# Kernel tuning notes

Measured on AMD Instinct MI355X. Metric: run time of the kernel, lower is better.

The kernel has to match this reference:

```python
import jax, jax.numpy as jnp
import numpy as np

N = 8192      # nodes (N_features)
D = 64        # oscillator dimension
E_K = 262144  # Kuramoto coupling edges
E_HK = 262144 # Hopfield-Kuramoto coupling edges
H = 64        # interaction MLP hidden width (N_weights)
KAPPA_K = 2.0
KAPPA_H = 2.0


def setup_inputs() -> dict:
    key = jax.random.key(0)
    ks = jax.random.split(key, 9)
    return dict(
        state_H=jax.random.normal(ks[0], (N,), dtype=jnp.float32),
        state_K=jax.random.normal(ks[1], (N, D), dtype=jnp.float32),
        W_H=jax.random.normal(ks[2], (N, N), dtype=jnp.float32) / np.float32(np.sqrt(N)),
        omega=jax.random.normal(ks[3], (D, D), dtype=jnp.float32),
        w1=jax.random.normal(ks[4], (1, H), dtype=jnp.float32),
        b1=jnp.zeros((H,), dtype=jnp.float32),
        w2=jax.random.normal(ks[5], (H, 1), dtype=jnp.float32) / np.float32(np.sqrt(H)),
        ind_K=jax.random.randint(ks[6], (E_K, 2), 0, N),
        ind_HK=jax.random.randint(ks[7], (E_HK, 2), 0, N),
    )


def _interaction_K(s, w1, b1, w2):
    # edgewise scalar MLP: [E] -> [E], dE/ds of the Kuramoto interaction energy
    h = jnp.tanh(s[:, None] @ w1 + b1)  # [E, H]
    return (h @ w2)[:, 0]               # [E]


def reference(state_H, state_K, W_H, omega, w1, b1, w2, ind_K, ind_HK):
    # normalize oscillator states onto unit sphere (per node)
    state_K = state_K / jnp.linalg.norm(state_K, axis=1, keepdims=True)

    i, j = ind_HK[:, 0], ind_HK[:, 1]
    Gram = jnp.sum(state_K[i] * state_K[j], axis=1)  # [E_HK]

    # Hopfield model: g = LNet.get_g(state_H), f_H = Hopfield_model(t, state_H, ...)
    g = jnp.tanh(state_H)                 # [N]
    f_H = -state_H + W_H @ g              # [N] dense Hopfield dynamics
    f_H = f_H.at[i].add(Gram * g[j] / KAPPA_H)
    f_H = f_H.at[j].add(Gram * g[i] / KAPPA_H)

    # Kuramoto edge coupling
    p, q = ind_K[:, 0], ind_K[:, 1]
    s = jnp.sum(state_K[p] * state_K[q], axis=1)        # [E_K]
    dE_ds = _interaction_K(s, w1, b1, w2)[:, None]      # [E_K, 1]
    f_K = jnp.zeros_like(state_K)
    f_K = f_K.at[p].add(dE_ds * state_K[q])
    f_K = f_K.at[q].add(dE_ds * state_K[p])

    # Hopfield->Kuramoto coupling
    G = (g[i] * g[j])[:, None]                          # [E_HK, 1]
    f_K = f_K.at[i].add(-G * state_K[j] / KAPPA_K)
    f_K = f_K.at[j].add(-G * state_K[i] / KAPPA_K)

    # project onto tangent of the sphere + antisymmetric rotation
    f_K = (-f_K
           + state_K * jnp.sum(state_K * f_K, axis=1, keepdims=True)
           + state_K @ ((omega - omega.T) * 0.5))
    return (f_H, f_K)
```

## Files before the change

kernel.cpp:

```cpp
#include <hip/hip_runtime.h>
#include <math.h>

#define N 8192
#define D 64
#define E_K 262144
#define E_HK 262144
#define NEDGE (E_K + E_HK)
#define CAP 256
#define TAB_N 2048

__device__ inline float fast_tanh(float x) {
  x = fminf(15.f, fmaxf(-15.f, x));
  float e = __expf(2.f * x);
  return (e - 1.f) * __builtin_amdgcn_rcpf(e + 1.f);
}

__device__ inline float wave_reduce(float v) {
  #pragma unroll
  for (int off = 32; off > 0; off >>= 1) v += __shfl_xor(v, off);
  return v;
}

__global__ __launch_bounds__(256) void prep_scatter_kernel(
    const float* __restrict__ state_K, const float* __restrict__ state_H,
    const float* __restrict__ omega,
    const int* __restrict__ ind_HK, const int* __restrict__ ind_K,
    const float* __restrict__ w1, const float* __restrict__ b1,
    const float* __restrict__ w2,
    float* __restrict__ Knorm, float* __restrict__ g, float* __restrict__ Om,
    float* __restrict__ Tab, int* __restrict__ cursor,
    unsigned* __restrict__ entries) {
  int b = blockIdx.x;
  if (b < 2048) {
    int t = b * 256 + threadIdx.x;
    int2 e = (t < E_HK) ? ((const int2*)ind_HK)[t]
                        : ((const int2*)ind_K)[t - E_HK];
    unsigned i = (unsigned)e.x, j = (unsigned)e.y;
    int s0 = atomicAdd(&cursor[i], 1);
    if (s0 < CAP) entries[i * CAP + s0] = (j << 19) | (unsigned)t;
    int s1 = atomicAdd(&cursor[j], 1);
    if (s1 < CAP) entries[j * CAP + s1] = (i << 19) | (unsigned)t;
  } else if (b < 4096) {
    int lane = threadIdx.x & 63;
    int row  = (b - 2048) * 4 + (threadIdx.x >> 6);
    float v  = state_K[row * D + lane];
    float ss = wave_reduce(v * v);
    Knorm[row * D + lane] = v * __builtin_amdgcn_rcpf(sqrtf(ss));
    if (lane == 0) g[row] = fast_tanh(state_H[row]);
  } else if (b == 4096) {
    for (int t = threadIdx.x; t < D * D; t += 256) {
      int a = t >> 6, c = t & 63;
      Om[t] = 0.5f * (omega[a * D + c] - omega[c * D + a]);
    }
  } else {
    int lane = threadIdx.x & 63;
    int p = (b - 4097) * 4 + (threadIdx.x >> 6);
    if (p <= TAB_N) {
      float s = (float)p * (2.0f / TAB_N) - 1.0f;
      float t = fast_tanh(s * w1[lane] + b1[lane]) * w2[lane];
      t = wave_reduce(t);
      if (lane == 0) Tab[p] = t;
    }
  }
}

__global__ __launch_bounds__(256) void matvec_coeff_kernel(
    const float* __restrict__ W_H, const float* __restrict__ g,
    const float* __restrict__ state_H, const float* __restrict__ Knorm,
    const float* __restrict__ Tab,
    const int* __restrict__ ind_HK, const int* __restrict__ ind_K,
    float* __restrict__ f_H, float* __restrict__ coeff) {
  int b    = blockIdx.x;
  int lane = threadIdx.x & 63;
  int wv   = threadIdx.x >> 6;
  __shared__ float sbuf[4];
  if (b < N) {
    int row = b;
    const float4* Wrow = reinterpret_cast<const float4*>(W_H + (size_t)row * N);
    const float4* g4   = reinterpret_cast<const float4*>(g);
    float acc = 0.0f;
    #pragma unroll
    for (int c = threadIdx.x; c < N / 4; c += 256) {
      float4 w = Wrow[c];
      float4 gg = g4[c];
      acc += w.x * gg.x + w.y * gg.y + w.z * gg.z + w.w * gg.w;
    }
    acc = wave_reduce(acc);
    if (lane == 0) sbuf[wv] = acc;
    __syncthreads();
    if (threadIdx.x == 0)
      f_H[row] = -state_H[row] + sbuf[0] + sbuf[1] + sbuf[2] + sbuf[3];
  } else {
    int wid = (b - N) * 4 + wv;
    int2 e = (wid < E_HK) ? ((const int2*)ind_HK)[wid]
                          : ((const int2*)ind_K)[wid - E_HK];
    float kp = Knorm[e.x * D + lane];
    float kq = Knorm[e.y * D + lane];
    float s = wave_reduce(kp * kq);
    float c = s;
    if (wid >= E_HK) {
      float x = fminf(fmaxf((s + 1.0f) * (TAB_N * 0.5f), 0.0f), (float)TAB_N);
      int   i  = min((int)x, TAB_N - 1);
      float fr = x - (float)i;
      c = Tab[i] + (Tab[i + 1] - Tab[i]) * fr;
    }
    if (lane == 0) coeff[wid] = c;
  }
}

__global__ __launch_bounds__(256) void gather_kernel(
    const float* __restrict__ Knorm, const float* __restrict__ g,
    const float* __restrict__ Om, const float* __restrict__ coeff,
    const int* __restrict__ cursor, const unsigned* __restrict__ entries,
    float* __restrict__ f_H, float* __restrict__ f_K) {
  int row  = blockIdx.x;
  int lane = threadIdx.x & 63;
  int wv   = threadIdx.x >> 6;
  float kr = Knorm[row * D + lane];
  float gr = g[row];
  int len  = min(cursor[row], CAP);

  int slot = lane * 4 + wv;
  unsigned myent = (unsigned)E_HK;
  float myc = 0.f, myg = 0.f;
  if (slot < len) {
    myent = entries[(size_t)row * CAP + slot];
    myc   = coeff[myent & 0x7FFFFu];
    myg   = g[myent >> 19];
  }
  int nl = (len > wv) ? min(64, (len - wv + 3) >> 2) : 0;

  float acc = 0.f, sH = 0.f;
  for (int k = 0; k < nl; k += 4) {
    #pragma unroll
    for (int u = 0; u < 4; ++u) {
      unsigned ent = (unsigned)__shfl((int)myent, k + u);
      float c  = __shfl(myc, k + u);
      float go = __shfl(myg, k + u);
      unsigned oth = ent >> 19;
      bool hk = (ent & 0x7FFFFu) < (unsigned)E_HK;
      float ko = Knorm[oth * D + lane];
      acc += (hk ? (-gr * go * 0.5f) : c) * ko;
      sH  += hk ? c * go : 0.f;
    }
  }

  __shared__ float sAcc[4][D];
  __shared__ float sHs[4];
  sAcc[wv][lane] = acc;
  if (lane == 0) sHs[wv] = sH;
  __syncthreads();
  if (wv == 0) {
    float tot = sAcc[0][lane] + sAcc[1][lane] + sAcc[2][lane] + sAcc[3][lane];
    float rd = wave_reduce(kr * tot);
    float krot = 0.f;
    #pragma unroll
    for (int d = 0; d < D; ++d)
      krot += __shfl(kr, d) * Om[d * D + lane];
    f_K[row * D + lane] = -tot + kr * rd + krot;
    if (lane == 0)
      f_H[row] += (sHs[0] + sHs[1] + sHs[2] + sHs[3]) * 0.5f;
  }
}

extern "C" void kernel_launch(void* const* d_in, const int* in_sizes, int n_in,
                              void* d_out, int out_size, void* d_ws, size_t ws_size,
                              hipStream_t stream) {
  const float* state_H = (const float*)d_in[0];
  const float* state_K = (const float*)d_in[1];
  const float* W_H     = (const float*)d_in[2];
  const float* omega   = (const float*)d_in[3];
  const float* w1      = (const float*)d_in[4];
  const float* b1      = (const float*)d_in[5];
  const float* w2      = (const float*)d_in[6];
  const int*   ind_K   = (const int*)d_in[7];
  const int*   ind_HK  = (const int*)d_in[8];

  float* f_H = (float*)d_out;
  float* f_K = (float*)d_out + N;

  char* ws = (char*)d_ws;
  unsigned* entries = (unsigned*)ws;     ws += (size_t)N * CAP * sizeof(unsigned);
  float* Knorm  = (float*)ws;            ws += (size_t)N * D * sizeof(float);
  float* coeff  = (float*)ws;            ws += (size_t)NEDGE * sizeof(float);
  float* g      = (float*)ws;            ws += N * sizeof(float);
  float* Om     = (float*)ws;            ws += D * D * sizeof(float);
  float* Tab    = (float*)ws;            ws += (TAB_N + 1) * sizeof(float);
  int*   cursor = (int*)ws;

  hipMemsetAsync(cursor, 0, N * sizeof(int), stream);
  prep_scatter_kernel<<<4097 + 513, 256, 0, stream>>>(
      state_K, state_H, omega, ind_HK, ind_K, w1, b1, w2,
      Knorm, g, Om, Tab, cursor, entries);
  matvec_coeff_kernel<<<N + NEDGE / 4, 256, 0, stream>>>(
      W_H, g, state_H, Knorm, Tab, ind_HK, ind_K, f_H, coeff);
  gather_kernel<<<N, 256, 0, stream>>>(Knorm, g, Om, coeff, cursor, entries,
                                       f_H, f_K);
}
```

Before: 563.2 us.

## Split matvec and edge coefficients into separate kernels with thread-per-edge dots

```diff
diff --git a/kernel.cpp b/kernel.cpp
--- a/kernel.cpp
+++ b/kernel.cpp
@@ -64,48 +64,50 @@
   }
 }
 
-__global__ __launch_bounds__(256) void matvec_coeff_kernel(
+__global__ __launch_bounds__(256) void coeff_kernel(
+    const float* __restrict__ Knorm, const float* __restrict__ Tab,
+    const int* __restrict__ ind_HK, const int* __restrict__ ind_K,
+    float* __restrict__ coeff) {
+  int t = blockIdx.x * 256 + threadIdx.x;
+  int2 e = (t < E_HK) ? ((const int2*)ind_HK)[t]
+                      : ((const int2*)ind_K)[t - E_HK];
+  const float4* rp = reinterpret_cast<const float4*>(Knorm + (size_t)e.x * D);
+  const float4* rq = reinterpret_cast<const float4*>(Knorm + (size_t)e.y * D);
+  float s = 0.f;
+  #pragma unroll
+  for (int d4 = 0; d4 < 16; ++d4) {
+    float4 a = rp[d4], b = rq[d4];
+    s += a.x * b.x + a.y * b.y + a.z * b.z + a.w * b.w;
+  }
+  float c = s;
+  if (t >= E_HK) {
+    float x = fminf(fmaxf((s + 1.0f) * (TAB_N * 0.5f), 0.0f), (float)TAB_N);
+    int   i  = min((int)x, TAB_N - 1);
+    float fr = x - (float)i;
+    c = Tab[i] + (Tab[i + 1] - Tab[i]) * fr;
+  }
+  coeff[t] = c;
+}
+
+__global__ __launch_bounds__(256) void matvec_kernel(
     const float* __restrict__ W_H, const float* __restrict__ g,
-    const float* __restrict__ state_H, const float* __restrict__ Knorm,
-    const float* __restrict__ Tab,
-    const int* __restrict__ ind_HK, const int* __restrict__ ind_K,
-    float* __restrict__ f_H, float* __restrict__ coeff) {
-  int b    = blockIdx.x;
+    const float* __restrict__ state_H, float* __restrict__ f_H) {
   int lane = threadIdx.x & 63;
-  int wv   = threadIdx.x >> 6;
-  __shared__ float sbuf[4];
-  if (b < N) {
-    int row = b;
-    const float4* Wrow = reinterpret_cast<const float4*>(W_H + (size_t)row * N);
-    const float4* g4   = reinterpret_cast<const float4*>(g);
-    float acc = 0.0f;
+  int row  = blockIdx.x * 4 + (threadIdx.x >> 6);
+  const float4* Wrow = reinterpret_cast<const float4*>(W_H + (size_t)row * N);
+  const float4* g4   = reinterpret_cast<const float4*>(g);
+  float acc = 0.f;
+  #pragma unroll 4
+  for (int o = 0; o < 32; o += 8) {
     #pragma unroll
-    for (int c = threadIdx.x; c < N / 4; c += 256) {
-      float4 w = Wrow[c];
-      float4 gg = g4[c];
+    for (int k = 0; k < 8; ++k) {
+      float4 w  = Wrow[lane + (o + k) * 64];
+      float4 gg = g4[lane + (o + k) * 64];
       acc += w.x * gg.x + w.y * gg.y + w.z * gg.z + w.w * gg.w;
     }
-    acc = wave_reduce(acc);
-    if (lane == 0) sbuf[wv] = acc;
-    __syncthreads();
-    if (threadIdx.x == 0)
-      f_H[row] = -state_H[row] + sbuf[0] + sbuf[1] + sbuf[2] + sbuf[3];
-  } else {
-    int wid = (b - N) * 4 + wv;
-    int2 e = (wid < E_HK) ? ((const int2*)ind_HK)[wid]
-                          : ((const int2*)ind_K)[wid - E_HK];
-    float kp = Knorm[e.x * D + lane];
-    float kq = Knorm[e.y * D + lane];
-    float s = wave_reduce(kp * kq);
-    float c = s;
-    if (wid >= E_HK) {
-      float x = fminf(fmaxf((s + 1.0f) * (TAB_N * 0.5f), 0.0f), (float)TAB_N);
-      int   i  = min((int)x, TAB_N - 1);
-      float fr = x - (float)i;
-      c = Tab[i] + (Tab[i + 1] - Tab[i]) * fr;
-    }
-    if (lane == 0) coeff[wid] = c;
-  }
+  }
+  acc = wave_reduce(acc);
+  if (lane == 0) f_H[row] = -state_H[row] + acc;
 }
 
 __global__ __launch_bounds__(256) void gather_kernel(
@@ -192,8 +194,9 @@
   prep_scatter_kernel<<<4097 + 513, 256, 0, stream>>>(
       state_K, state_H, omega, ind_HK, ind_K, w1, b1, w2,
       Knorm, g, Om, Tab, cursor, entries);
-  matvec_coeff_kernel<<<N + NEDGE / 4, 256, 0, stream>>>(
-      W_H, g, state_H, Knorm, Tab, ind_HK, ind_K, f_H, coeff);
+  coeff_kernel<<<NEDGE / 256, 256, 0, stream>>>(Knorm, Tab, ind_HK, ind_K,
+                                                coeff);
+  matvec_kernel<<<N / 4, 256, 0, stream>>>(W_H, g, state_H, f_H);
   gather_kernel<<<N, 256, 0, stream>>>(Knorm, g, Om, coeff, cursor, entries,
                                        f_H, f_K);
 }
```

Result: faster. 514.4 us (-8.7%).
